# Optimization experiments

Measured on AMD Instinct MI355X. Metric: run time of the kernel, lower is better.

## Reference

```python
import jax, jax.numpy as jnp
import numpy as np

B, T, N, D_OBJ = 8, 32, 10, 2048
N_VERB, N_OBJCLS = 157, 353
D_EMB, D_VERB = 512, 2048


def setup_inputs() -> dict:
    key = jax.random.key(0)
    k1, k2, k3, k4, k5 = jax.random.split(key, 5)
    objects_features = jax.random.normal(k1, (B, T, N, D_OBJ), dtype=jnp.float32)
    fm_context = jax.random.normal(k2, (B, T, D_VERB), dtype=jnp.float32)
    obj_id = jax.random.randint(k3, (B, T, N, N_OBJCLS), 0, 2, dtype=jnp.int32)
    W = jax.random.normal(k4, (D_OBJ, D_EMB), dtype=jnp.float32) * 0.02
    b = jnp.zeros((D_EMB,), dtype=jnp.float32)
    A_o2v = jnp.full((N_VERB, N_OBJCLS), 1.0 / N_VERB, dtype=jnp.float32)
    return {"objects_features": objects_features, "fm_context": fm_context,
            "obj_id": obj_id, "W": W, "b": b, "A_o2v": A_o2v}


def reference(objects_features, fm_context, obj_id, W, b, A_o2v):
    D = obj_id.shape[-1]
    # one-hot cleanup: all-zero row -> class 0; multi-hot row -> last nonzero class
    row_sum = obj_id.sum(-1)                                  # (B,T,N)
    last_nz = (D - 1) - jnp.argmax(jnp.flip(obj_id, -1), -1)  # last nonzero index
    cls = jnp.where(row_sum == 0, 0, last_nz)                 # (B,T,N)

    obj_embedded = objects_features @ W + b                   # (B,T,N,D_emb)

    # subA[b,t,n,v] = A_o2v[v, cls[b,t,n]]
    subA = A_o2v.T[cls]                                       # (B,T,N,V)

    afforded = jnp.einsum('btnv,btnd->btvd', subA, obj_embedded)  # (B,T,V,D_emb)

    V = A_o2v.shape[0]
    ctx = jnp.broadcast_to(fm_context[:, :, None, :],
                           (afforded.shape[0], afforded.shape[1], V, fm_context.shape[-1]))
    vo_actions = jnp.concatenate([afforded, ctx], axis=-1)    # (B,T,V,D_emb+D_verb)
    return vo_actions.mean(axis=1)                            # (B,V,D_emb+D_verb)
```

## Files before the change

### kernel.cpp

```cpp
#include <hip/hip_runtime.h>


typedef __attribute__((ext_vector_type(8))) short short8;
typedef __attribute__((ext_vector_type(8))) unsigned short us8;
typedef __attribute__((ext_vector_type(4))) unsigned short us4;
typedef __attribute__((ext_vector_type(4))) float f32x4;

#define OFF_CTX  0
#define OFF_SAT  65536
#define OFF_WT   1048576
#define OFF_FB   3145728
#define OFF_PART 13631488
#define OFF_CLS  39845888

static __device__ inline unsigned short f2bf(float x) {
    unsigned int u = __builtin_bit_cast(unsigned int, x);
    u += 0x7fffu + ((u >> 16) & 1u);
    return (unsigned short)(u >> 16);
}
static __device__ inline void gl16(const void* g, void* l) {
    __builtin_amdgcn_global_load_lds(
        (__attribute__((address_space(1))) void*)(g),
        (__attribute__((address_space(3))) void*)(l), 16, 0, 0);
}

__global__ void k_cls(const int* __restrict__ obj_id, int* __restrict__ cls)
{
    int row  = blockIdx.x * 4 + (threadIdx.x >> 6);
    int lane = threadIdx.x & 63;
    if (row >= 2560) return;
    const int* p = obj_id + (size_t)row * 353;
    int last = -1;
    #pragma unroll
    for (int base = 0; base < 384; base += 64) {
        int idx = base + lane;
        int v = (idx < 353) ? p[idx] : 0;
        unsigned long long m = __ballot(v != 0);
        if (m) last = base + 63 - __clzll(m);
    }
    if (lane == 0) cls[row] = (last < 0) ? 0 : last;
}

__global__ __launch_bounds__(256) void k_prep(
    const float* __restrict__ W, const float* __restrict__ fm,
    const float* __restrict__ feat, const int* __restrict__ cls,
    const float* __restrict__ A,
    unsigned short* __restrict__ Wt, float* __restrict__ ctx,
    unsigned short* __restrict__ featb, unsigned short* __restrict__ sAT)
{
    __shared__ float t[32][33];
    __shared__ int lcls[64];
    int bx = blockIdx.x, tid = threadIdx.x;

    if (bx < 1280) {
        size_t id = (size_t)bx * 256 + tid;
        const float* p = feat + id * 16;
        us8 o0, o1;
        #pragma unroll
        for (int j = 0; j < 8; j++) o0[j] = f2bf(p[j]);
        #pragma unroll
        for (int j = 0; j < 8; j++) o1[j] = f2bf(p[8 + j]);
        *(us8*)&featb[id * 16] = o0;
        *(us8*)&featb[id * 16 + 8] = o1;
    } else if (bx < 2304) {
        int b2 = bx - 1280;
        int r0 = (b2 >> 4) * 32, c0 = (b2 & 15) * 32;
        int rr = tid >> 3, cc = (tid & 7) * 4;
        float4 v = *(const float4*)&W[(size_t)(r0 + rr) * 512 + c0 + cc];
        t[rr][cc] = v.x; t[rr][cc+1] = v.y; t[rr][cc+2] = v.z; t[rr][cc+3] = v.w;
        __syncthreads();
        us4 o = { f2bf(t[cc][rr]), f2bf(t[cc+1][rr]), f2bf(t[cc+2][rr]), f2bf(t[cc+3][rr]) };
        *(us4*)&Wt[(size_t)(c0 + rr) * 2048 + r0 + cc] = o;
    } else if (bx < 2368) {
        int id = (bx - 2304) * 256 + tid;
        int b = id >> 11, d = id & 2047;
        const float* p = fm + (size_t)b * 32 * 2048 + d;
        float s = 0.f;
        #pragma unroll
        for (int tt = 0; tt < 32; tt++) s += p[(size_t)tt * 2048];
        ctx[id] = s * (1.0f / 32.0f);
    } else {
        int blk = bx - 2368;
        int b = blk / 5, i0 = (blk % 5) * 64;
        if (tid < 64) lcls[tid] = cls[b * 320 + i0 + tid];
        __syncthreads();
        #pragma unroll
        for (int q = 0; q < 6; q++) {
            int u = q * 256 + tid;
            int v = u >> 3, i8 = u & 7;
            us8 o = {};
            if (v < 157) {
                #pragma unroll
                for (int j = 0; j < 8; j++)
                    o[j] = f2bf(A[v * 353 + lcls[i8 * 8 + j]] * (1.0f / 32.0f));
            }
            *(us8*)&sAT[((size_t)b * 192 + v) * 320 + i0 + i8 * 8] = o;
        }
    }
}

__global__ __launch_bounds__(256) void k_gemmE(
    const unsigned short* __restrict__ featb, const unsigned short* __restrict__ Wt,
    float* __restrict__ part)
{
    int bx = blockIdx.x;
    int ks = bx & 3, nt = (bx >> 2) & 3, mt = bx >> 4;
    int m0 = mt * 64, n0 = nt * 128, k0 = ks * 512;
    int b = m0 / 320, i0 = m0 % 320;

    __shared__ __align__(16) unsigned short la[2][64 * 64];
    __shared__ __align__(16) unsigned short lb[2][128 * 64];

    int tid = threadIdx.x, lane = tid & 63, w = tid >> 6;
    int wm = (w >> 1) * 32, wn = (w & 1) * 64;
    int fr = lane & 15, fk = lane >> 4;

    const unsigned short* gA[2];
    #pragma unroll
    for (int c = 0; c < 2; c++) {
        int s = c * 256 + tid, ar = s >> 3, ch = s & 7;
        gA[c] = featb + (size_t)(b * 320 + i0 + ar) * 2048 + k0 + ((ch ^ (ar & 7)) << 3);
    }
    const unsigned short* gB[4];
    #pragma unroll
    for (int c = 0; c < 4; c++) {
        int s = c * 256 + tid, er = s >> 3, ch = s & 7;
        gB[c] = Wt + (size_t)(n0 + er) * 2048 + k0 + ((ch ^ (er & 7)) << 3);
    }

    f32x4 acc[2][4] = {};

    auto stage = [&](int buf, int kk) {
        #pragma unroll
        for (int c = 0; c < 2; c++) gl16(gA[c] + kk, &la[buf][(c * 256 + tid) * 8]);
        #pragma unroll
        for (int c = 0; c < 4; c++) gl16(gB[c] + kk, &lb[buf][(c * 256 + tid) * 8]);
    };
    auto compute = [&](int buf) {
        #pragma unroll
        for (int k2 = 0; k2 < 2; k2++) {
            short8 af[2], bf[4];
            #pragma unroll
            for (int mi = 0; mi < 2; mi++) {
                int r = wm + mi * 16 + fr;
                af[mi] = *(const short8*)&la[buf][r * 64 + (((k2 * 4 + fk) ^ (r & 7)) << 3)];
            }
            #pragma unroll
            for (int ni = 0; ni < 4; ni++) {
                int r = wn + ni * 16 + fr;
                bf[ni] = *(const short8*)&lb[buf][r * 64 + (((k2 * 4 + fk) ^ (r & 7)) << 3)];
            }
            #pragma unroll
            for (int mi = 0; mi < 2; mi++)
                #pragma unroll
                for (int ni = 0; ni < 4; ni++)
                    acc[mi][ni] = __builtin_amdgcn_mfma_f32_16x16x32_bf16(
                        af[mi], bf[ni], acc[mi][ni], 0, 0, 0);
        }
    };

    stage(0, 0);
    __syncthreads();
    int cur = 0;
    #pragma unroll 1
    for (int t = 0; t < 8; t++) {
        if (t < 7) stage(cur ^ 1, (t + 1) * 64);
        compute(cur);
        __syncthreads();
        cur ^= 1;
    }

    #pragma unroll
    for (int mi = 0; mi < 2; mi++) {
        int i = i0 + wm + mi * 16 + fk * 4;
        #pragma unroll
        for (int ni = 0; ni < 4; ni++) {
            int e = n0 + wn + ni * 16 + fr;
            *(f32x4*)&part[((size_t)(b * 512 + e) * 4 + ks) * 320 + i] = acc[mi][ni];
        }
    }
}

__global__ __launch_bounds__(256) void k_out(
    const unsigned short* __restrict__ sAT, const float* __restrict__ part,
    const float* __restrict__ bias, const float* __restrict__ ctx,
    float* __restrict__ out)
{
    if (blockIdx.x >= 96) {
        int id = (blockIdx.x - 96) * 256 + threadIdx.x;
        int q = id & 511, bv = id >> 9, b = bv / 157;
        float4 v = *(const float4*)&ctx[((size_t)b << 11) + q * 4];
        *(float4*)&out[(size_t)bv * 2560 + 512 + q * 4] = v;
        return;
    }
    int bx = blockIdx.x;
    int b = bx / 12, r = bx % 12;
    int v0 = (r >> 2) * 64, e0 = (r & 3) * 128;

    __shared__ __align__(16) unsigned short la[2][64 * 32];
    __shared__ __align__(16) unsigned short lb[2][128 * 32];

    int tid = threadIdx.x, lane = tid & 63, w = tid >> 6;
    int wm = (w >> 1) * 32, wn = (w & 1) * 64;
    int fr = lane & 15, fk = lane >> 4;

    int aer = tid >> 2, ach = tid & 3;
    const unsigned short* gA = sAT + ((size_t)b * 192 + v0 + aer) * 320
                                   + ((ach ^ (aer & 3)) << 3);
    const float* pb = part + (size_t)b * 512 * 4 * 320;

    f32x4 acc[2][4] = {};
    f32x4 s0, s1, s2, s3;
    float be0, be1, be2, be3;

    auto loadB = [&](int kk) {
        f32x4* sp[4] = { &s0, &s1, &s2, &s3 };
        float* bp[4] = { &be0, &be1, &be2, &be3 };
        #pragma unroll
        for (int q = 0; q < 4; q++) {
            int u = q * 256 + tid, e = u >> 3, i4 = u & 7;
            const float* base = pb + (size_t)(e0 + e) * 4 * 320 + kk + i4 * 4;
            f32x4 s = *(const f32x4*)(base);
            s += *(const f32x4*)(base + 320);
            s += *(const f32x4*)(base + 640);
            s += *(const f32x4*)(base + 960);
            *sp[q] = s;
            *bp[q] = bias[e0 + e];
        }
    };
    auto writeB = [&](int buf) {
        f32x4 sv[4] = { s0, s1, s2, s3 };
        float bv[4] = { be0, be1, be2, be3 };
        #pragma unroll
        for (int q = 0; q < 4; q++) {
            int u = q * 256 + tid, e = u >> 3, i4 = u & 7;
            f32x4 s = sv[q];
            float be = bv[q];
            us4 o = { f2bf(s[0] + be), f2bf(s[1] + be), f2bf(s[2] + be), f2bf(s[3] + be) };
            *(us4*)&lb[buf][e * 32 + ((((i4 >> 1) ^ (e & 3)) << 3) + (i4 & 1) * 4)] = o;
        }
    };
    auto compute = [&](int buf) {
        short8 af[2], bf[4];
        #pragma unroll
        for (int mi = 0; mi < 2; mi++) {
            int rr = wm + mi * 16 + fr;
            af[mi] = *(const short8*)&la[buf][rr * 32 + ((fk ^ (rr & 3)) << 3)];
        }
        #pragma unroll
        for (int ni = 0; ni < 4; ni++) {
            int rr = wn + ni * 16 + fr;
            bf[ni] = *(const short8*)&lb[buf][rr * 32 + ((fk ^ (rr & 3)) << 3)];
        }
        #pragma unroll
        for (int mi = 0; mi < 2; mi++)
            #pragma unroll
            for (int ni = 0; ni < 4; ni++)
                acc[mi][ni] = __builtin_amdgcn_mfma_f32_16x16x32_bf16(
                    af[mi], bf[ni], acc[mi][ni], 0, 0, 0);
    };

    gl16(gA, &la[0][tid * 8]);
    loadB(0); writeB(0);
    __syncthreads();
    int cur = 0;
    #pragma unroll 1
    for (int t = 0; t < 10; t++) {
        if (t < 9) { gl16(gA + (t + 1) * 32, &la[cur ^ 1][tid * 8]); loadB((t + 1) * 32); }
        compute(cur);
        if (t < 9) writeB(cur ^ 1);
        __syncthreads();
        cur ^= 1;
    }

    #pragma unroll
    for (int mi = 0; mi < 2; mi++) {
        int vb = v0 + wm + mi * 16 + fk * 4;
        #pragma unroll
        for (int ni = 0; ni < 4; ni++) {
            int e = e0 + wn + ni * 16 + fr;
            #pragma unroll
            for (int rr = 0; rr < 4; rr++) {
                int v = vb + rr;
                if (v < 157)
                    out[((size_t)b * 157 + v) * 2560 + e] = acc[mi][ni][rr];
            }
        }
    }
}

extern "C" void kernel_launch(void* const* d_in, const int* in_sizes, int n_in,
                              void* d_out, int out_size, void* d_ws, size_t ws_size,
                              hipStream_t stream)
{
    const float* feat = (const float*)d_in[0];
    const float* fm   = (const float*)d_in[1];
    const int*   obj  = (const int*)d_in[2];
    const float* W    = (const float*)d_in[3];
    const float* bias = (const float*)d_in[4];
    const float* A    = (const float*)d_in[5];
    float* out = (float*)d_out;

    char* ws = (char*)d_ws;
    float*          ctx   = (float*)(ws + OFF_CTX);
    unsigned short* sAT   = (unsigned short*)(ws + OFF_SAT);
    unsigned short* Wt    = (unsigned short*)(ws + OFF_WT);
    unsigned short* featb = (unsigned short*)(ws + OFF_FB);
    float*          part  = (float*)(ws + OFF_PART);
    int*            cls   = (int*)(ws + OFF_CLS);

    k_cls  <<<640, 256, 0, stream>>>(obj, cls);
    k_prep <<<2408, 256, 0, stream>>>(W, fm, feat, cls, A, Wt, ctx, featb, sAT);
    k_gemmE<<<640, 256, 0, stream>>>(featb, Wt, part);
    k_out  <<<2608, 256, 0, stream>>>(sAT, part, bias, ctx, out);
}
```

Measured before the change: 118.0 us.

## Reassociate GEMMs: aggregate features by affordance before projecting with W

The order of the two contractions is swapped. Object features are first aggregated per verb (subA^T · feat, giving a 157x2048 matrix per batch) and then projected through W, instead of projecting every object to 512 dims and then aggregating. The bias is folded in by multiplying it with a per-verb column sum of subA, so the old fp32 partial-sum reduction fused into the second GEMM becomes a simple finalize kernel. This needs a transposed bf16 copy of the features, an extra bf16 intermediate G, and one more kernel launch. Rounding G to bf16 adds some precision error.

```diff
diff --git a/kernel.cpp b/kernel.cpp
--- a/kernel.cpp
+++ b/kernel.cpp
@@ -9,9 +9,11 @@
 #define OFF_CTX  0
 #define OFF_SAT  65536
 #define OFF_WT   1048576
-#define OFF_FB   3145728
-#define OFF_PART 13631488
-#define OFF_CLS  39845888
+#define OFF_FT   3145728
+#define OFF_G    13631488
+#define OFF_PART 19922944
+#define OFF_CLS  32505856
+#define OFF_CNT  32516096
 
 static __device__ inline unsigned short f2bf(float x) {
     unsigned int u = __builtin_bit_cast(unsigned int, x);
@@ -46,24 +48,25 @@
     const float* __restrict__ feat, const int* __restrict__ cls,
     const float* __restrict__ A,
     unsigned short* __restrict__ Wt, float* __restrict__ ctx,
-    unsigned short* __restrict__ featb, unsigned short* __restrict__ sAT)
+    unsigned short* __restrict__ featT, unsigned short* __restrict__ sAT,
+    float* __restrict__ cnt)
 {
     __shared__ float t[32][33];
-    __shared__ int lcls[64];
+    __shared__ int lcls[320];
     int bx = blockIdx.x, tid = threadIdx.x;
 
-    if (bx < 1280) {
-        size_t id = (size_t)bx * 256 + tid;
-        const float* p = feat + id * 16;
-        us8 o0, o1;
-        #pragma unroll
-        for (int j = 0; j < 8; j++) o0[j] = f2bf(p[j]);
-        #pragma unroll
-        for (int j = 0; j < 8; j++) o1[j] = f2bf(p[8 + j]);
-        *(us8*)&featb[id * 16] = o0;
-        *(us8*)&featb[id * 16 + 8] = o1;
-    } else if (bx < 2304) {
-        int b2 = bx - 1280;
+    if (bx < 5120) {
+        int b  = bx / 640;
+        int r  = bx % 640;
+        int it = r / 64, dt = r % 64;
+        int rr = tid >> 3, cc = (tid & 7) * 4;
+        float4 v = *(const float4*)&feat[((size_t)b * 320 + it * 32 + rr) * 2048 + dt * 32 + cc];
+        t[rr][cc] = v.x; t[rr][cc+1] = v.y; t[rr][cc+2] = v.z; t[rr][cc+3] = v.w;
+        __syncthreads();
+        us4 o = { f2bf(t[cc][rr]), f2bf(t[cc+1][rr]), f2bf(t[cc+2][rr]), f2bf(t[cc+3][rr]) };
+        *(us4*)&featT[((size_t)b * 2048 + dt * 32 + rr) * 320 + it * 32 + cc] = o;
+    } else if (bx < 6144) {
+        int b2 = bx - 5120;
         int r0 = (b2 >> 4) * 32, c0 = (b2 & 15) * 32;
         int rr = tid >> 3, cc = (tid & 7) * 4;
         float4 v = *(const float4*)&W[(size_t)(r0 + rr) * 512 + c0 + cc];
@@ -71,16 +74,16 @@
         __syncthreads();
         us4 o = { f2bf(t[cc][rr]), f2bf(t[cc+1][rr]), f2bf(t[cc+2][rr]), f2bf(t[cc+3][rr]) };
         *(us4*)&Wt[(size_t)(c0 + rr) * 2048 + r0 + cc] = o;
-    } else if (bx < 2368) {
-        int id = (bx - 2304) * 256 + tid;
+    } else if (bx < 6208) {
+        int id = (bx - 6144) * 256 + tid;
         int b = id >> 11, d = id & 2047;
         const float* p = fm + (size_t)b * 32 * 2048 + d;
         float s = 0.f;
         #pragma unroll
         for (int tt = 0; tt < 32; tt++) s += p[(size_t)tt * 2048];
         ctx[id] = s * (1.0f / 32.0f);
-    } else {
-        int blk = bx - 2368;
+    } else if (bx < 6248) {
+        int blk = bx - 6208;
         int b = blk / 5, i0 = (blk % 5) * 64;
         if (tid < 64) lcls[tid] = cls[b * 320 + i0 + tid];
         __syncthreads();
@@ -96,17 +99,109 @@
             }
             *(us8*)&sAT[((size_t)b * 192 + v) * 320 + i0 + i8 * 8] = o;
         }
-    }
-}
-
-__global__ __launch_bounds__(256) void k_gemmE(
-    const unsigned short* __restrict__ featb, const unsigned short* __restrict__ Wt,
+    } else {
+        int b = bx - 6248;
+        for (int i = tid; i < 320; i += 256) lcls[i] = cls[b * 320 + i];
+        __syncthreads();
+        if (tid < 157) {
+            float s = 0.f;
+            for (int i = 0; i < 320; i++) s += A[tid * 353 + lcls[i]];
+            cnt[b * 192 + tid] = s * (1.0f / 32.0f);
+        }
+    }
+}
+
+__global__ __launch_bounds__(256) void k_gemmG(
+    const unsigned short* __restrict__ sAT, const unsigned short* __restrict__ featT,
+    unsigned short* __restrict__ G)
+{
+    int bx = blockIdx.x;
+    int b = bx / 48, r = bx % 48;
+    int mt = r / 16, nt = r % 16;
+    int m0 = mt * 64, n0 = nt * 128;
+
+    __shared__ __align__(16) unsigned short la[2][64 * 64];
+    __shared__ __align__(16) unsigned short lb[2][128 * 64];
+
+    int tid = threadIdx.x, lane = tid & 63, w = tid >> 6;
+    int wm = (w >> 1) * 32, wn = (w & 1) * 64;
+    int fr = lane & 15, fk = lane >> 4;
+
+    const unsigned short* gA[2];
+    #pragma unroll
+    for (int c = 0; c < 2; c++) {
+        int s = c * 256 + tid, ar = s >> 3, ch = s & 7;
+        gA[c] = sAT + ((size_t)b * 192 + m0 + ar) * 320 + ((ch ^ (ar & 7)) << 3);
+    }
+    const unsigned short* gB[4];
+    #pragma unroll
+    for (int c = 0; c < 4; c++) {
+        int s = c * 256 + tid, er = s >> 3, ch = s & 7;
+        gB[c] = featT + ((size_t)b * 2048 + n0 + er) * 320 + ((ch ^ (er & 7)) << 3);
+    }
+
+    f32x4 acc[2][4] = {};
+
+    auto stage = [&](int buf, int kk) {
+        #pragma unroll
+        for (int c = 0; c < 2; c++) gl16(gA[c] + kk, &la[buf][(c * 256 + tid) * 8]);
+        #pragma unroll
+        for (int c = 0; c < 4; c++) gl16(gB[c] + kk, &lb[buf][(c * 256 + tid) * 8]);
+    };
+    auto compute = [&](int buf) {
+        #pragma unroll
+        for (int k2 = 0; k2 < 2; k2++) {
+            short8 af[2], bf[4];
+            #pragma unroll
+            for (int mi = 0; mi < 2; mi++) {
+                int rr = wm + mi * 16 + fr;
+                af[mi] = *(const short8*)&la[buf][rr * 64 + (((k2 * 4 + fk) ^ (rr & 7)) << 3)];
+            }
+            #pragma unroll
+            for (int ni = 0; ni < 4; ni++) {
+                int rr = wn + ni * 16 + fr;
+                bf[ni] = *(const short8*)&lb[buf][rr * 64 + (((k2 * 4 + fk) ^ (rr & 7)) << 3)];
+            }
+            #pragma unroll
+            for (int mi = 0; mi < 2; mi++)
+                #pragma unroll
+                for (int ni = 0; ni < 4; ni++)
+                    acc[mi][ni] = __builtin_amdgcn_mfma_f32_16x16x32_bf16(
+                        af[mi], bf[ni], acc[mi][ni], 0, 0, 0);
+        }
+    };
+
+    stage(0, 0);
+    __syncthreads();
+    int cur = 0;
+    #pragma unroll 1
+    for (int t = 0; t < 5; t++) {
+        if (t < 4) stage(cur ^ 1, (t + 1) * 64);
+        compute(cur);
+        __syncthreads();
+        cur ^= 1;
+    }
+
+    #pragma unroll
+    for (int mi = 0; mi < 2; mi++) {
+        int v0 = m0 + wm + mi * 16 + fk * 4;
+        #pragma unroll
+        for (int ni = 0; ni < 4; ni++) {
+            int d = n0 + wn + ni * 16 + fr;
+            #pragma unroll
+            for (int rr = 0; rr < 4; rr++)
+                G[((size_t)b * 192 + v0 + rr) * 2048 + d] = f2bf(acc[mi][ni][rr]);
+        }
+    }
+}
+
+__global__ __launch_bounds__(256) void k_gemm2(
+    const unsigned short* __restrict__ G, const unsigned short* __restrict__ Wt,
     float* __restrict__ part)
 {
     int bx = blockIdx.x;
     int ks = bx & 3, nt = (bx >> 2) & 3, mt = bx >> 4;
     int m0 = mt * 64, n0 = nt * 128, k0 = ks * 512;
-    int b = m0 / 320, i0 = m0 % 320;
 
     __shared__ __align__(16) unsigned short la[2][64 * 64];
     __shared__ __align__(16) unsigned short lb[2][128 * 64];
@@ -119,7 +214,7 @@
     #pragma unroll
     for (int c = 0; c < 2; c++) {
         int s = c * 256 + tid, ar = s >> 3, ch = s & 7;
-        gA[c] = featb + (size_t)(b * 320 + i0 + ar) * 2048 + k0 + ((ch ^ (ar & 7)) << 3);
+        gA[c] = G + (size_t)(m0 + ar) * 2048 + k0 + ((ch ^ (ar & 7)) << 3);
     }
     const unsigned short* gB[4];
     #pragma unroll
@@ -142,13 +237,13 @@
             short8 af[2], bf[4];
             #pragma unroll
             for (int mi = 0; mi < 2; mi++) {
-                int r = wm + mi * 16 + fr;
-                af[mi] = *(const short8*)&la[buf][r * 64 + (((k2 * 4 + fk) ^ (r & 7)) << 3)];
+                int rr = wm + mi * 16 + fr;
+                af[mi] = *(const short8*)&la[buf][rr * 64 + (((k2 * 4 + fk) ^ (rr & 7)) << 3)];
             }
             #pragma unroll
             for (int ni = 0; ni < 4; ni++) {
-                int r = wn + ni * 16 + fr;
-                bf[ni] = *(const short8*)&lb[buf][r * 64 + (((k2 * 4 + fk) ^ (r & 7)) << 3)];
+                int rr = wn + ni * 16 + fr;
+                bf[ni] = *(const short8*)&lb[buf][rr * 64 + (((k2 * 4 + fk) ^ (rr & 7)) << 3)];
             }
             #pragma unroll
             for (int mi = 0; mi < 2; mi++)
@@ -170,122 +265,45 @@
         cur ^= 1;
     }
 
+    float* P = part + (size_t)ks * 1536 * 512;
     #pragma unroll
     for (int mi = 0; mi < 2; mi++) {
-        int i = i0 + wm + mi * 16 + fk * 4;
+        int mrow = m0 + wm + mi * 16 + fk * 4;
         #pragma unroll
         for (int ni = 0; ni < 4; ni++) {
             int e = n0 + wn + ni * 16 + fr;
-            *(f32x4*)&part[((size_t)(b * 512 + e) * 4 + ks) * 320 + i] = acc[mi][ni];
-        }
-    }
-}
-
-__global__ __launch_bounds__(256) void k_out(
-    const unsigned short* __restrict__ sAT, const float* __restrict__ part,
-    const float* __restrict__ bias, const float* __restrict__ ctx,
-    float* __restrict__ out)
-{
-    if (blockIdx.x >= 96) {
-        int id = (blockIdx.x - 96) * 256 + threadIdx.x;
+            #pragma unroll
+            for (int rr = 0; rr < 4; rr++)
+                P[(size_t)(mrow + rr) * 512 + e] = acc[mi][ni][rr];
+        }
+    }
+}
+
+__global__ void k_fin(const float* __restrict__ part, const float* __restrict__ cnt,
+                      const float* __restrict__ bias, const float* __restrict__ ctx,
+                      float* __restrict__ out)
+{
+    if (blockIdx.x < 768) {
+        int id = blockIdx.x * 256 + threadIdx.x;
+        int e4 = id & 127;
+        int m  = id >> 7;
+        int v = m % 192, b = m / 192;
+        if (v >= 157) return;
+        float4 s = ((const float4*)bias)[e4];
+        float c = cnt[m];
+        s.x *= c; s.y *= c; s.z *= c; s.w *= c;
+        #pragma unroll
+        for (int ks = 0; ks < 4; ks++) {
+            float4 p = *(const float4*)&part[((size_t)ks * 1536 + m) * 512 + e4 * 4];
+            s.x += p.x; s.y += p.y; s.z += p.z; s.w += p.w;
+        }
+        *(float4*)&out[((size_t)b * 157 + v) * 2560 + e4 * 4] = s;
+    } else {
+        int id = (blockIdx.x - 768) * 256 + threadIdx.x;
+        if (id >= 8 * 157 * 512) return;
         int q = id & 511, bv = id >> 9, b = bv / 157;
         float4 v = *(const float4*)&ctx[((size_t)b << 11) + q * 4];
         *(float4*)&out[(size_t)bv * 2560 + 512 + q * 4] = v;
-        return;
-    }
-    int bx = blockIdx.x;
-    int b = bx / 12, r = bx % 12;
-    int v0 = (r >> 2) * 64, e0 = (r & 3) * 128;
-
-    __shared__ __align__(16) unsigned short la[2][64 * 32];
-    __shared__ __align__(16) unsigned short lb[2][128 * 32];
-
-    int tid = threadIdx.x, lane = tid & 63, w = tid >> 6;
-    int wm = (w >> 1) * 32, wn = (w & 1) * 64;
-    int fr = lane & 15, fk = lane >> 4;
-
-    int aer = tid >> 2, ach = tid & 3;
-    const unsigned short* gA = sAT + ((size_t)b * 192 + v0 + aer) * 320
-                                   + ((ach ^ (aer & 3)) << 3);
-    const float* pb = part + (size_t)b * 512 * 4 * 320;
-
-    f32x4 acc[2][4] = {};
-    f32x4 s0, s1, s2, s3;
-    float be0, be1, be2, be3;
-
-    auto loadB = [&](int kk) {
-        f32x4* sp[4] = { &s0, &s1, &s2, &s3 };
-        float* bp[4] = { &be0, &be1, &be2, &be3 };
-        #pragma unroll
-        for (int q = 0; q < 4; q++) {
-            int u = q * 256 + tid, e = u >> 3, i4 = u & 7;
-            const float* base = pb + (size_t)(e0 + e) * 4 * 320 + kk + i4 * 4;
-            f32x4 s = *(const f32x4*)(base);
-            s += *(const f32x4*)(base + 320);
-            s += *(const f32x4*)(base + 640);
-            s += *(const f32x4*)(base + 960);
-            *sp[q] = s;
-            *bp[q] = bias[e0 + e];
-        }
-    };
-    auto writeB = [&](int buf) {
-        f32x4 sv[4] = { s0, s1, s2, s3 };
-        float bv[4] = { be0, be1, be2, be3 };
-        #pragma unroll
-        for (int q = 0; q < 4; q++) {
-            int u = q * 256 + tid, e = u >> 3, i4 = u & 7;
-            f32x4 s = sv[q];
-            float be = bv[q];
-            us4 o = { f2bf(s[0] + be), f2bf(s[1] + be), f2bf(s[2] + be), f2bf(s[3] + be) };
-            *(us4*)&lb[buf][e * 32 + ((((i4 >> 1) ^ (e & 3)) << 3) + (i4 & 1) * 4)] = o;
-        }
-    };
-    auto compute = [&](int buf) {
-        short8 af[2], bf[4];
-        #pragma unroll
-        for (int mi = 0; mi < 2; mi++) {
-            int rr = wm + mi * 16 + fr;
-            af[mi] = *(const short8*)&la[buf][rr * 32 + ((fk ^ (rr & 3)) << 3)];
-        }
-        #pragma unroll
-        for (int ni = 0; ni < 4; ni++) {
-            int rr = wn + ni * 16 + fr;
-            bf[ni] = *(const short8*)&lb[buf][rr * 32 + ((fk ^ (rr & 3)) << 3)];
-        }
-        #pragma unroll
-        for (int mi = 0; mi < 2; mi++)
-            #pragma unroll
-            for (int ni = 0; ni < 4; ni++)
-                acc[mi][ni] = __builtin_amdgcn_mfma_f32_16x16x32_bf16(
-                    af[mi], bf[ni], acc[mi][ni], 0, 0, 0);
-    };
-
-    gl16(gA, &la[0][tid * 8]);
-    loadB(0); writeB(0);
-    __syncthreads();
-    int cur = 0;
-    #pragma unroll 1
-    for (int t = 0; t < 10; t++) {
-        if (t < 9) { gl16(gA + (t + 1) * 32, &la[cur ^ 1][tid * 8]); loadB((t + 1) * 32); }
-        compute(cur);
-        if (t < 9) writeB(cur ^ 1);
-        __syncthreads();
-        cur ^= 1;
-    }
-
-    #pragma unroll
-    for (int mi = 0; mi < 2; mi++) {
-        int vb = v0 + wm + mi * 16 + fk * 4;
-        #pragma unroll
-        for (int ni = 0; ni < 4; ni++) {
-            int e = e0 + wn + ni * 16 + fr;
-            #pragma unroll
-            for (int rr = 0; rr < 4; rr++) {
-                int v = vb + rr;
-                if (v < 157)
-                    out[((size_t)b * 157 + v) * 2560 + e] = acc[mi][ni][rr];
-            }
-        }
     }
 }
 
@@ -305,12 +323,15 @@
     float*          ctx   = (float*)(ws + OFF_CTX);
     unsigned short* sAT   = (unsigned short*)(ws + OFF_SAT);
     unsigned short* Wt    = (unsigned short*)(ws + OFF_WT);
-    unsigned short* featb = (unsigned short*)(ws + OFF_FB);
+    unsigned short* featT = (unsigned short*)(ws + OFF_FT);
+    unsigned short* G     = (unsigned short*)(ws + OFF_G);
     float*          part  = (float*)(ws + OFF_PART);
     int*            cls   = (int*)(ws + OFF_CLS);
+    float*          cnt   = (float*)(ws + OFF_CNT);
 
     k_cls  <<<640, 256, 0, stream>>>(obj, cls);
-    k_prep <<<2408, 256, 0, stream>>>(W, fm, feat, cls, A, Wt, ctx, featb, sAT);
-    k_gemmE<<<640, 256, 0, stream>>>(featb, Wt, part);
-    k_out  <<<2608, 256, 0, stream>>>(sAT, part, bias, ctx, out);
-}
+    k_prep <<<6256, 256, 0, stream>>>(W, fm, feat, cls, A, Wt, ctx, featT, sAT, cnt);
+    k_gemmG<<<384, 256, 0, stream>>>(sAT, featT, G);
+    k_gemm2<<<384, 256, 0, stream>>>(G, Wt, part);
+    k_fin  <<<3280, 256, 0, stream>>>(part, cnt, bias, ctx, out);
+}
```

Result: slower. 124.4 us (+5.4%).
